# Kernel tuning notes

Hardware: AMD Instinct MI355X
Metric: run time of the kernel (lower is better)

Reference implementation:

```python
import jax, jax.numpy as jnp
import numpy as np

B, C, H, W = 2, 128, 64, 64
NUM_HEADS = 8
GN_GROUPS = 8
GN_EPS = 1e-5


def setup_inputs() -> dict:
    key = jax.random.key(0)
    ks = jax.random.split(key, 11)
    s = 0.02
    return {
        "x": jax.random.normal(ks[0], (B, C, H, W), dtype=jnp.float32),
        "Wq": jax.random.normal(ks[1], (C, C), dtype=jnp.float32) * s,
        "bq": jnp.zeros((C,), dtype=jnp.float32),
        "Wk": jax.random.normal(ks[2], (C, C), dtype=jnp.float32) * s,
        "bk": jnp.zeros((C,), dtype=jnp.float32),
        "Wv": jax.random.normal(ks[3], (C, C), dtype=jnp.float32) * s,
        "bv": jnp.zeros((C,), dtype=jnp.float32),
        "Wo": jax.random.normal(ks[4], (C, C), dtype=jnp.float32) * s,
        "bo": jnp.zeros((C,), dtype=jnp.float32),
        "gn_w": jnp.ones((C,), dtype=jnp.float32),
        "gn_b": jnp.zeros((C,), dtype=jnp.float32),
    }


def reference(x, Wq, bq, Wk, bk, Wv, bv, Wo, bo, gn_w, gn_b):
    b, c, h, w = x.shape
    nh = NUM_HEADS
    dh = c // nh
    scale = dh ** (-0.5)

    # [b, c, h, w] -> [b, N, c]
    x_seq = x.reshape(b, c, h * w).transpose(0, 2, 1)

    def proj(W, bias):
        y = jnp.einsum('bnc,dc->bnd', x_seq, W) + bias  # nn.Linear: x @ W.T + b
        return y.reshape(b, -1, nh, dh).transpose(0, 2, 1, 3)  # [b, nh, N, dh]

    q = proj(Wq, bq)
    k = proj(Wk, bk)
    v = proj(Wv, bv)

    attn = jnp.einsum('bhnd,bhmd->bhnm', q, k) * scale  # [b, nh, N, N]
    attn = jax.nn.softmax(attn, axis=-1)
    out = jnp.einsum('bhnm,bhmd->bhnd', attn, v)        # [b, nh, N, dh]

    out = out.transpose(0, 2, 1, 3).reshape(b, -1, c)   # [b, N, c]
    out = jnp.einsum('bnc,dc->bnd', out, Wo) + bo
    out = out.transpose(0, 2, 1).reshape(b, c, h, w)

    # GroupNorm(8, c) with affine params, then residual
    g = GN_GROUPS
    og = out.reshape(b, g, c // g, h, w)
    mean = jnp.mean(og, axis=(2, 3, 4), keepdims=True)
    var = jnp.var(og, axis=(2, 3, 4), keepdims=True)
    og = (og - mean) * jax.lax.rsqrt(var + GN_EPS)
    normed = og.reshape(b, c, h, w) * gn_w[None, :, None, None] + gn_b[None, :, None, None]
    return normed + x
```

## Files before the change

kernel.cpp:

```cpp
#include <hip/hip_runtime.h>

#define TID ((int)threadIdx.x)

constexpr int Bb  = 2;
constexpr int Cc  = 128;
constexpr int Nn  = 4096;
constexpr int NHh = 8;
constexpr int DHd = 16;
constexpr int NSP = 4;
constexpr float GN_EPS_F = 1e-5f;
constexpr float QSCALE = 0.25f * 1.4426950408889634f;

typedef float  f32x4  __attribute__((ext_vector_type(4)));
typedef float  f32x16 __attribute__((ext_vector_type(16)));
typedef short  s16x8  __attribute__((ext_vector_type(8)));
typedef unsigned short u16x8 __attribute__((ext_vector_type(8)));

#if __has_builtin(__builtin_amdgcn_exp2f)
#define EXP2(x) __builtin_amdgcn_exp2f(x)
#else
#define EXP2(x) exp2f(x)
#endif

constexpr size_t WS_PART = 0;
constexpr size_t WS_LP   = 4096;
constexpr size_t WS_AOP  = WS_LP + (size_t)NSP*16*Nn;
constexpr size_t WS_QBF  = WS_AOP + ((size_t)NSP*Bb*Nn*Cc)/2;
constexpr size_t BF_ELEMS = (size_t)Bb*NHh*Nn*DHd;
constexpr size_t WS_W    = WS_QBF + 3*(BF_ELEMS/2);

__device__ __forceinline__ ushort f2bf(float f) {
    uint u = __builtin_bit_cast(uint, f);
    u += 0x7fffu + ((u >> 16) & 1u);
    return (ushort)(u >> 16);
}
__device__ __forceinline__ float bf2f(ushort u) {
    return __builtin_bit_cast(float, ((uint)u) << 16);
}
__device__ __forceinline__ uint cvt_pk_bf16(float lo, float hi) {
    uint d;
    asm("v_cvt_pk_bf16_f32 %0, %1, %2" : "=v"(d) : "v"(lo), "v"(hi));
    return d;
}

__global__ __launch_bounds__(256) void prep_w_kernel(
    const float* __restrict__ Wq, const float* __restrict__ Wk,
    const float* __restrict__ Wv, const float* __restrict__ Wo,
    ushort* __restrict__ wh, ushort* __restrict__ wl)
{
    int id = blockIdx.x * 256 + TID;
    int which = id >> 14, i = id & 16383;
    const float* src = (which == 0) ? Wq : (which == 1) ? Wk : (which == 2) ? Wv : Wo;
    float v = src[i];
    if (which == 0) v *= QSCALE;
    ushort h = f2bf(v);
    ushort l = f2bf(v - bf2f(h));
    wh[id] = h;
    wl[id] = l;
}

__global__ __launch_bounds__(256) void qkv_kernel(
    const float* __restrict__ x,
    const float* __restrict__ bq, const float* __restrict__ bk, const float* __restrict__ bv,
    const ushort* __restrict__ wh, const ushort* __restrict__ wl,
    ushort* __restrict__ qbf, ushort* __restrict__ kbf, ushort* __restrict__ vtbf)
{
    const int b  = blockIdx.x >> 7;
    const int n0 = (blockIdx.x & 127) << 5;
    __shared__ __align__(16) ushort xh[32][136];
    __shared__ __align__(16) ushort xl[32][136];

    const float* xb = x + (size_t)b * Cc * Nn;
    {
        int c = TID >> 1, nh2 = (TID & 1) * 16;
#pragma unroll
        for (int j = 0; j < 4; ++j) {
            float4 v4 = *(const float4*)&xb[(size_t)c * Nn + n0 + nh2 + 4*j];
            float f[4] = {v4.x, v4.y, v4.z, v4.w};
#pragma unroll
            for (int e = 0; e < 4; ++e) {
                int n = nh2 + 4*j + e;
                ushort h = f2bf(f[e]);
                xh[n][c] = h;
                xl[n][c] = f2bf(f[e] - bf2f(h));
            }
        }
    }
    __syncthreads();

    const int lane = TID & 63, wave = TID >> 6;
    const int l31 = lane & 31, hi = lane >> 5;
    const int d0 = wave * 32;

    const ushort* wqh = wh;              const ushort* wql = wl;
    const ushort* wkh = wh + 16384;      const ushort* wkl = wl + 16384;
    const ushort* wvh = wh + 2 * 16384;  const ushort* wvl = wl + 2 * 16384;

    f32x16 qacc = (f32x16)(0.f), kacc = (f32x16)(0.f);
    f32x16 vacc = (f32x16)(bv[d0 + l31]);
    const size_t wrow = (size_t)(d0 + l31) * 128;

#pragma unroll 2
    for (int ks = 0; ks < 8; ++ks) {
        const int co = ks * 16 + 8 * hi;
        s16x8 xhf = *(const s16x8*)&xh[l31][co];
        s16x8 xlf = *(const s16x8*)&xl[l31][co];
        s16x8 aqh = *(const s16x8*)(wqh + wrow + co);
        s16x8 aql = *(const s16x8*)(wql + wrow + co);
        s16x8 akh = *(const s16x8*)(wkh + wrow + co);
        s16x8 akl = *(const s16x8*)(wkl + wrow + co);
        s16x8 avh = *(const s16x8*)(wvh + wrow + co);
        s16x8 avl = *(const s16x8*)(wvl + wrow + co);
        qacc = __builtin_amdgcn_mfma_f32_32x32x16_bf16(aqh, xhf, qacc, 0, 0, 0);
        qacc = __builtin_amdgcn_mfma_f32_32x32x16_bf16(aql, xhf, qacc, 0, 0, 0);
        qacc = __builtin_amdgcn_mfma_f32_32x32x16_bf16(aqh, xlf, qacc, 0, 0, 0);
        kacc = __builtin_amdgcn_mfma_f32_32x32x16_bf16(akh, xhf, kacc, 0, 0, 0);
        kacc = __builtin_amdgcn_mfma_f32_32x32x16_bf16(akl, xhf, kacc, 0, 0, 0);
        kacc = __builtin_amdgcn_mfma_f32_32x32x16_bf16(akh, xlf, kacc, 0, 0, 0);
        vacc = __builtin_amdgcn_mfma_f32_32x32x16_bf16(xhf, avh, vacc, 0, 0, 0);
        vacc = __builtin_amdgcn_mfma_f32_32x32x16_bf16(xhf, avl, vacc, 0, 0, 0);
        vacc = __builtin_amdgcn_mfma_f32_32x32x16_bf16(xlf, avh, vacc, 0, 0, 0);
    }

    {
        const int n = n0 + l31;
#pragma unroll
        for (int q = 0; q < 4; ++q) {
            const int dbase = d0 + 8*q + 4*hi;
            const int h = dbase >> 4, dh0 = dbase & 15;
            float4 bq4 = *(const float4*)&bq[dbase];
            float4 bk4 = *(const float4*)&bk[dbase];
            uint2 wq2, wk2;
            wq2.x = cvt_pk_bf16(qacc[4*q+0] + bq4.x * QSCALE, qacc[4*q+1] + bq4.y * QSCALE);
            wq2.y = cvt_pk_bf16(qacc[4*q+2] + bq4.z * QSCALE, qacc[4*q+3] + bq4.w * QSCALE);
            wk2.x = cvt_pk_bf16(kacc[4*q+0] + bk4.x, kacc[4*q+1] + bk4.y);
            wk2.y = cvt_pk_bf16(kacc[4*q+2] + bk4.z, kacc[4*q+3] + bk4.w);
            size_t base = ((size_t)((b*NHh + h) * Nn + n)) * DHd + dh0;
            *(uint2*)(qbf + base) = wq2;
            *(uint2*)(kbf + base) = wk2;
        }
    }
    {
        const int d = d0 + l31;
        const int h = d >> 4, dd = d & 15;
        ushort* vrow = vtbf + ((size_t)(b*NHh + h) * DHd + dd) * Nn;
#pragma unroll
        for (int q = 0; q < 4; ++q) {
            uint2 w2;
            w2.x = cvt_pk_bf16(vacc[4*q+0], vacc[4*q+1]);
            w2.y = cvt_pk_bf16(vacc[4*q+2], vacc[4*q+3]);
            *(uint2*)(vrow + n0 + 8*q + 4*hi) = w2;
        }
    }
}

__global__ __launch_bounds__(256, 5) void attn_kernel(
    const ushort* __restrict__ qbf, const ushort* __restrict__ kbf,
    const ushort* __restrict__ vtbf, ushort* __restrict__ aop, float* __restrict__ lp)
{
    const int qt = blockIdx.x & 31;
    const int sp = (blockIdx.x >> 5) & 3;
    const int bh = blockIdx.x >> 7;
    const int q0 = qt << 7;
    const int kvbase = sp << 10;
    const ushort* qb  = qbf  + (size_t)bh * Nn * DHd;
    const ushort* kb  = kbf  + (size_t)bh * Nn * DHd;
    const ushort* vtb = vtbf + (size_t)bh * DHd * Nn;

    __shared__ __align__(16) ushort k_lds[64][16];
    __shared__ __align__(16) ushort vt_lds[16][88];
    __shared__ __align__(16) ushort ps[4][32][88];

    const int wave = TID >> 6, lane = TID & 63;
    const int l31 = lane & 31, hi = lane >> 5;
    const int l15 = lane & 15, g  = lane >> 4;
    const int wq = q0 + wave * 32;

    const s16x8 qfrag = *(const s16x8*)(qb + (size_t)(wq + l31) * DHd + 8 * hi);

    float l_run = 0.0f;
    f32x4 o0 = (f32x4)(0.f), o1 = (f32x4)(0.f);
    ushort* psw = &ps[wave][0][0];

    for (int kv0 = kvbase; kv0 < kvbase + 1024; kv0 += 64) {
        if (TID < 128) {
            *(u16x8*)((char*)&k_lds[0][0] + TID * 16) =
                *(const u16x8*)(kb + (size_t)kv0 * DHd + TID * 8);
        } else {
            int t = TID - 128, r = t >> 3, c8 = (t & 7) * 8;
            *(u16x8*)&vt_lds[r][c8] = *(const u16x8*)(vtb + (size_t)r * Nn + kv0 + c8);
        }
        __syncthreads();

        s16x8 af0 = *(const s16x8*)&k_lds[l31][8 * hi];
        s16x8 af1 = *(const s16x8*)&k_lds[32 + l31][8 * hi];
        f32x16 st0 = __builtin_amdgcn_mfma_f32_32x32x16_bf16(af0, qfrag, (f32x16)(0.f), 0, 0, 0);
        f32x16 st1 = __builtin_amdgcn_mfma_f32_32x32x16_bf16(af1, qfrag, (f32x16)(0.f), 0, 0, 0);

        float rs = 0.f;
        {
            float p[16];
#pragma unroll
            for (int r = 0; r < 16; ++r) { p[r] = EXP2(st0[r]); rs += p[r]; }
            char* rowp = (char*)psw + (size_t)l31 * 176;
#pragma unroll
            for (int m4 = 0; m4 < 4; ++m4) {
                uint2 w;
                w.x = cvt_pk_bf16(p[4*m4 + 0], p[4*m4 + 1]);
                w.y = cvt_pk_bf16(p[4*m4 + 2], p[4*m4 + 3]);
                *(uint2*)(rowp + 16*m4 + 8*hi) = w;
            }
        }
        {
            float p[16];
#pragma unroll
            for (int r = 0; r < 16; ++r) { p[r] = EXP2(st1[r]); rs += p[r]; }
            char* rowp = (char*)psw + (size_t)l31 * 176;
#pragma unroll
            for (int m4 = 0; m4 < 4; ++m4) {
                uint2 w;
                w.x = cvt_pk_bf16(p[4*m4 + 0], p[4*m4 + 1]);
                w.y = cvt_pk_bf16(p[4*m4 + 2], p[4*m4 + 3]);
                *(uint2*)(rowp + 16*m4 + 8*hi + 64) = w;
            }
        }
        l_run += rs;

#pragma unroll
        for (int cc = 0; cc < 2; ++cc) {
            s16x8 vf  = *(const s16x8*)&vt_lds[l15][cc*32 + 8*g];
            s16x8 pf0 = *(const s16x8*)((char*)psw + (size_t)l15 * 176        + 16*g + 64*cc);
            s16x8 pf1 = *(const s16x8*)((char*)psw + (size_t)(16 + l15) * 176 + 16*g + 64*cc);
            o0 = __builtin_amdgcn_mfma_f32_16x16x32_bf16(pf0, vf, o0, 0, 0, 0);
            o1 = __builtin_amdgcn_mfma_f32_16x16x32_bf16(pf1, vf, o1, 0, 0, 0);
        }
        __syncthreads();
    }

    l_run += __shfl_xor(l_run, 32, 64);
    if (hi == 0)
        lp[((size_t)(sp * 16 + bh)) * Nn + wq + l31] = l_run;

    const int b = bh >> 3, hh = bh & 7;
    ushort* ap = aop + (((size_t)(sp * Bb + b)) * Nn) * Cc;
#pragma unroll
    for (int r = 0; r < 4; ++r) {
        int n0r = wq + 4*g + r, n1r = wq + 16 + 4*g + r;
        ap[(size_t)n0r * Cc + hh * DHd + l15] = f2bf(o0[r]);
        ap[(size_t)n1r * Cc + hh * DHd + l15] = f2bf(o1[r]);
    }
}

__global__ __launch_bounds__(256) void oproj_kernel(
    const ushort* __restrict__ aop, const float* __restrict__ lp,
    const ushort* __restrict__ wh, const ushort* __restrict__ wl,
    const float* __restrict__ bo,
    float* __restrict__ y, float* __restrict__ partial)
{
    const int b  = blockIdx.x >> 7;
    const int nb = blockIdx.x & 127;
    const int n0 = nb << 5;
    __shared__ __align__(16) ushort aoc[32][136];
    __shared__ float linv[32][8];

    {
        int n = TID >> 3, h = TID & 7;
        float l = 0.f;
#pragma unroll
        for (int sp = 0; sp < NSP; ++sp)
            l += lp[((size_t)(sp * 16 + b * 8 + h)) * Nn + n0 + n];
        linv[n][h] = 1.0f / l;
    }
    __syncthreads();

#pragma unroll
    for (int s = TID; s < 512; s += 256) {
        int n = s >> 4, c8 = s & 15;
        int c = c8 * 8;
        float a[8];
#pragma unroll
        for (int e = 0; e < 8; ++e) a[e] = 0.f;
#pragma unroll
        for (int sp = 0; sp < NSP; ++sp) {
            u16x8 u = *(const u16x8*)(aop + (((size_t)(sp * Bb + b)) * Nn + n0 + n) * Cc + c);
#pragma unroll
            for (int e = 0; e < 8; ++e) a[e] += bf2f(u[e]);
        }
        float li = linv[n][c >> 4];
        uint4 w;
        w.x = cvt_pk_bf16(a[0]*li, a[1]*li);
        w.y = cvt_pk_bf16(a[2]*li, a[3]*li);
        w.z = cvt_pk_bf16(a[4]*li, a[5]*li);
        w.w = cvt_pk_bf16(a[6]*li, a[7]*li);
        *(uint4*)&aoc[n][c] = w;
    }
    __syncthreads();

    const int lane = TID & 63, wave = TID >> 6;
    const int l31 = lane & 31, hi = lane >> 5;
    const int d0 = wave * 32;
    const ushort* woh = wh + 3 * 16384;
    const ushort* wol = wl + 3 * 16384;
    const size_t wrow = (size_t)(d0 + l31) * 128;

    f32x16 acc = (f32x16)(bo[d0 + l31]);
#pragma unroll
    for (int ks = 0; ks < 8; ++ks) {
        const int co = ks * 16 + 8 * hi;
        s16x8 aof = *(const s16x8*)&aoc[l31][co];
        s16x8 bh8 = *(const s16x8*)(woh + wrow + co);
        s16x8 bl8 = *(const s16x8*)(wol + wrow + co);
        acc = __builtin_amdgcn_mfma_f32_32x32x16_bf16(aof, bh8, acc, 0, 0, 0);
        acc = __builtin_amdgcn_mfma_f32_32x32x16_bf16(aof, bl8, acc, 0, 0, 0);
    }

    const int d = d0 + l31;
    float* yrow = y + ((size_t)(b * Cc + d)) * Nn + n0;
    float s1 = 0.f, s2 = 0.f;
#pragma unroll
    for (int q = 0; q < 4; ++q) {
        float4 v4 = make_float4(acc[4*q+0], acc[4*q+1], acc[4*q+2], acc[4*q+3]);
        s1 += v4.x + v4.y + v4.z + v4.w;
        s2 += v4.x*v4.x + v4.y*v4.y + v4.z*v4.z + v4.w*v4.w;
        *(float4*)(yrow + 8*q + 4*hi) = v4;
    }
#pragma unroll
    for (int off = 1; off < 16; off <<= 1) {
        s1 += __shfl_xor(s1, off, 64);
        s2 += __shfl_xor(s2, off, 64);
    }
    s1 += __shfl_xor(s1, 32, 64);
    s2 += __shfl_xor(s2, 32, 64);
    if ((lane & 15) == 0 && hi == 0) {
        int g = d >> 4;
        float* p = partial + (((size_t)(b * 128 + nb)) * 8 + g) * 2;
        p[0] = s1; p[1] = s2;
    }
}

__global__ __launch_bounds__(256) void finalize_kernel(
    const float* __restrict__ x, const float* __restrict__ gn_w, const float* __restrict__ gn_b,
    const float* __restrict__ partial, float* __restrict__ out)
{
    __shared__ float red[4][2];
    const size_t i0 = (size_t)blockIdx.x << 10;
    const int b = (int)(i0 >> 19);
    const int c = (int)((i0 >> 12) & 127);
    const int g = c >> 4;

    float s1 = 0.f, s2 = 0.f;
    if (TID < 128) {
        const float* p = partial + (((size_t)(b * 128 + TID)) * 8 + g) * 2;
        s1 = p[0]; s2 = p[1];
    }
#pragma unroll
    for (int off = 1; off < 64; off <<= 1) {
        s1 += __shfl_xor(s1, off, 64);
        s2 += __shfl_xor(s2, off, 64);
    }
    if ((TID & 63) == 0) { red[TID >> 6][0] = s1; red[TID >> 6][1] = s2; }
    __syncthreads();
    s1 = red[0][0] + red[1][0] + red[2][0] + red[3][0];
    s2 = red[0][1] + red[1][1] + red[2][1] + red[3][1];

    const float inv_cnt = 1.0f / 65536.0f;
    float mean = s1 * inv_cnt;
    float var  = s2 * inv_cnt - mean * mean;
    float rstd = rsqrtf(var + GN_EPS_F);
    float a   = rstd * gn_w[c];
    float bb2 = gn_b[c] - mean * a;

    size_t i = i0 + (size_t)TID * 4;
    float4 yv = *(float4*)(out + i);
    float4 xv = *(const float4*)(x + i);
    float4 o;
    o.x = yv.x * a + bb2 + xv.x;
    o.y = yv.y * a + bb2 + xv.y;
    o.z = yv.z * a + bb2 + xv.z;
    o.w = yv.w * a + bb2 + xv.w;
    *(float4*)(out + i) = o;
}

extern "C" void kernel_launch(void* const* d_in, const int* in_sizes, int n_in,
                              void* d_out, int out_size, void* d_ws, size_t ws_size,
                              hipStream_t stream) {
    const float* x  = (const float*)d_in[0];
    const float* Wq = (const float*)d_in[1];
    const float* bq = (const float*)d_in[2];
    const float* Wk = (const float*)d_in[3];
    const float* bk = (const float*)d_in[4];
    const float* Wv = (const float*)d_in[5];
    const float* bv = (const float*)d_in[6];
    const float* Wo = (const float*)d_in[7];
    const float* bo = (const float*)d_in[8];
    const float* gw = (const float*)d_in[9];
    const float* gb = (const float*)d_in[10];
    float* out = (float*)d_out;
    float* ws  = (float*)d_ws;

    float*  partial = ws + WS_PART;
    float*  lpart   = ws + WS_LP;
    ushort* aop     = (ushort*)(ws + WS_AOP);
    ushort* qbf     = (ushort*)(ws + WS_QBF);
    ushort* kbf     = qbf + BF_ELEMS;
    ushort* vtbf    = kbf + BF_ELEMS;
    ushort* wh      = (ushort*)(ws + WS_W);
    ushort* wl      = wh + 4 * 16384;

    hipLaunchKernelGGL(prep_w_kernel, dim3(256), dim3(256), 0, stream,
                       Wq, Wk, Wv, Wo, wh, wl);
    hipLaunchKernelGGL(qkv_kernel, dim3(Bb * (Nn / 32)), dim3(256), 0, stream,
                       x, bq, bk, bv, wh, wl, qbf, kbf, vtbf);
    hipLaunchKernelGGL(attn_kernel, dim3(16 * NSP * 32), dim3(256), 0, stream,
                       qbf, kbf, vtbf, aop, lpart);
    hipLaunchKernelGGL(oproj_kernel, dim3(Bb * (Nn / 32)), dim3(256), 0, stream,
                       aop, lpart, wh, wl, bo, out, partial);
    hipLaunchKernelGGL(finalize_kernel, dim3((Bb * Cc * Nn) / 1024), dim3(256), 0, stream,
                       x, gw, gb, partial, out);
}
```

Measured before the change: 138.7 us.

## Keep P in registers via permlane32 swap and drop LDS staging in attention

The attention kernel no longer stages K, V^T and the probability tile through shared memory. It reads K and V fragments directly from global memory, rearranges the exponentiated scores across lane halves with v_permlane32_swap, and feeds them into 32x32x16 MFMAs that accumulate the transposed output. This removes the LDS writes and reads and both __syncthreads per tile. In exchange, every wave issues redundant global and cache loads and uses more accumulator registers, so launch bounds drop from 5 to 4 blocks per CU.

```diff
diff --git a/kernel.cpp b/kernel.cpp
--- a/kernel.cpp
+++ b/kernel.cpp
@@ -15,6 +15,7 @@
 typedef float  f32x16 __attribute__((ext_vector_type(16)));
 typedef short  s16x8  __attribute__((ext_vector_type(8)));
 typedef unsigned short u16x8 __attribute__((ext_vector_type(8)));
+typedef uint   u32x4  __attribute__((ext_vector_type(4)));
 
 #if __has_builtin(__builtin_amdgcn_exp2f)
 #define EXP2(x) __builtin_amdgcn_exp2f(x)
@@ -41,6 +42,13 @@
     uint d;
     asm("v_cvt_pk_bf16_f32 %0, %1, %2" : "=v"(d) : "v"(lo), "v"(hi));
     return d;
+}
+__device__ __forceinline__ void pl32swap(uint& a, uint& b) {
+    asm volatile("v_permlane32_swap_b32 %0, %1" : "+v"(a), "+v"(b));
+}
+__device__ __forceinline__ s16x8 pack4(uint a, uint b, uint c, uint d) {
+    u32x4 u; u[0] = a; u[1] = b; u[2] = c; u[3] = d;
+    return __builtin_bit_cast(s16x8, u);
 }
 
 __global__ __launch_bounds__(256) void prep_w_kernel(
@@ -154,7 +162,7 @@
     }
 }
 
-__global__ __launch_bounds__(256, 5) void attn_kernel(
+__global__ __launch_bounds__(256, 4) void attn_kernel(
     const ushort* __restrict__ qbf, const ushort* __restrict__ kbf,
     const ushort* __restrict__ vtbf, ushort* __restrict__ aop, float* __restrict__ lp)
 {
@@ -167,74 +175,52 @@
     const ushort* kb  = kbf  + (size_t)bh * Nn * DHd;
     const ushort* vtb = vtbf + (size_t)bh * DHd * Nn;
 
-    __shared__ __align__(16) ushort k_lds[64][16];
-    __shared__ __align__(16) ushort vt_lds[16][88];
-    __shared__ __align__(16) ushort ps[4][32][88];
-
-    const int wave = TID >> 6, lane = TID & 63;
+    const int lane = TID & 63, wave = TID >> 6;
     const int l31 = lane & 31, hi = lane >> 5;
-    const int l15 = lane & 15, g  = lane >> 4;
     const int wq = q0 + wave * 32;
 
     const s16x8 qfrag = *(const s16x8*)(qb + (size_t)(wq + l31) * DHd + 8 * hi);
 
     float l_run = 0.0f;
-    f32x4 o0 = (f32x4)(0.f), o1 = (f32x4)(0.f);
-    ushort* psw = &ps[wave][0][0];
+    f32x16 ot = (f32x16)(0.f);
+
+    const ushort* vrow = vtb + (size_t)(l31 & 15) * Nn + 8 * hi;
 
     for (int kv0 = kvbase; kv0 < kvbase + 1024; kv0 += 64) {
-        if (TID < 128) {
-            *(u16x8*)((char*)&k_lds[0][0] + TID * 16) =
-                *(const u16x8*)(kb + (size_t)kv0 * DHd + TID * 8);
-        } else {
-            int t = TID - 128, r = t >> 3, c8 = (t & 7) * 8;
-            *(u16x8*)&vt_lds[r][c8] = *(const u16x8*)(vtb + (size_t)r * Nn + kv0 + c8);
-        }
-        __syncthreads();
-
-        s16x8 af0 = *(const s16x8*)&k_lds[l31][8 * hi];
-        s16x8 af1 = *(const s16x8*)&k_lds[32 + l31][8 * hi];
+        const ushort* krow = kb + (size_t)kv0 * DHd + 8 * hi;
+        s16x8 af0 = *(const s16x8*)(krow + (size_t)l31 * DHd);
+        s16x8 af1 = *(const s16x8*)(krow + (size_t)(l31 + 32) * DHd);
         f32x16 st0 = __builtin_amdgcn_mfma_f32_32x32x16_bf16(af0, qfrag, (f32x16)(0.f), 0, 0, 0);
         f32x16 st1 = __builtin_amdgcn_mfma_f32_32x32x16_bf16(af1, qfrag, (f32x16)(0.f), 0, 0, 0);
 
         float rs = 0.f;
-        {
-            float p[16];
-#pragma unroll
-            for (int r = 0; r < 16; ++r) { p[r] = EXP2(st0[r]); rs += p[r]; }
-            char* rowp = (char*)psw + (size_t)l31 * 176;
-#pragma unroll
-            for (int m4 = 0; m4 < 4; ++m4) {
-                uint2 w;
-                w.x = cvt_pk_bf16(p[4*m4 + 0], p[4*m4 + 1]);
-                w.y = cvt_pk_bf16(p[4*m4 + 2], p[4*m4 + 3]);
-                *(uint2*)(rowp + 16*m4 + 8*hi) = w;
-            }
-        }
-        {
-            float p[16];
-#pragma unroll
-            for (int r = 0; r < 16; ++r) { p[r] = EXP2(st1[r]); rs += p[r]; }
-            char* rowp = (char*)psw + (size_t)l31 * 176;
-#pragma unroll
-            for (int m4 = 0; m4 < 4; ++m4) {
-                uint2 w;
-                w.x = cvt_pk_bf16(p[4*m4 + 0], p[4*m4 + 1]);
-                w.y = cvt_pk_bf16(p[4*m4 + 2], p[4*m4 + 3]);
-                *(uint2*)(rowp + 16*m4 + 8*hi + 64) = w;
-            }
-        }
+        uint p0,p1,p2,p3,p4,p5,p6,p7,p8,p9,p10,p11,p12,p13,p14,p15;
+#define PKE(dst, sreg, i0, i1) { float e0 = EXP2(sreg[i0]); float e1 = EXP2(sreg[i1]); \
+                                 rs += e0 + e1; dst = cvt_pk_bf16(e0, e1); }
+        PKE(p0,  st0,  0,  1)  PKE(p1,  st0,  2,  3)
+        PKE(p2,  st0,  4,  5)  PKE(p3,  st0,  6,  7)
+        PKE(p4,  st0,  8,  9)  PKE(p5,  st0, 10, 11)
+        PKE(p6,  st0, 12, 13)  PKE(p7,  st0, 14, 15)
+        PKE(p8,  st1,  0,  1)  PKE(p9,  st1,  2,  3)
+        PKE(p10, st1,  4,  5)  PKE(p11, st1,  6,  7)
+        PKE(p12, st1,  8,  9)  PKE(p13, st1, 10, 11)
+        PKE(p14, st1, 12, 13)  PKE(p15, st1, 14, 15)
+#undef PKE
+        pl32swap(p0,  p2);  pl32swap(p1,  p3);
+        pl32swap(p4,  p6);  pl32swap(p5,  p7);
+        pl32swap(p8,  p10); pl32swap(p9,  p11);
+        pl32swap(p12, p14); pl32swap(p13, p15);
+
+        s16x8 vf0 = *(const s16x8*)(vrow + kv0);
+        s16x8 vf1 = *(const s16x8*)(vrow + kv0 + 16);
+        s16x8 vf2 = *(const s16x8*)(vrow + kv0 + 32);
+        s16x8 vf3 = *(const s16x8*)(vrow + kv0 + 48);
+        ot = __builtin_amdgcn_mfma_f32_32x32x16_bf16(vf0, pack4(p0,p1,p2,p3),     ot, 0, 0, 0);
+        ot = __builtin_amdgcn_mfma_f32_32x32x16_bf16(vf1, pack4(p4,p5,p6,p7),     ot, 0, 0, 0);
+        ot = __builtin_amdgcn_mfma_f32_32x32x16_bf16(vf2, pack4(p8,p9,p10,p11),   ot, 0, 0, 0);
+        ot = __builtin_amdgcn_mfma_f32_32x32x16_bf16(vf3, pack4(p12,p13,p14,p15), ot, 0, 0, 0);
+
         l_run += rs;
-
-#pragma unroll
-        for (int cc = 0; cc < 2; ++cc) {
-            s16x8 vf  = *(const s16x8*)&vt_lds[l15][cc*32 + 8*g];
-            s16x8 pf0 = *(const s16x8*)((char*)psw + (size_t)l15 * 176        + 16*g + 64*cc);
-            s16x8 pf1 = *(const s16x8*)((char*)psw + (size_t)(16 + l15) * 176 + 16*g + 64*cc);
-            o0 = __builtin_amdgcn_mfma_f32_16x16x32_bf16(pf0, vf, o0, 0, 0, 0);
-            o1 = __builtin_amdgcn_mfma_f32_16x16x32_bf16(pf1, vf, o1, 0, 0, 0);
-        }
-        __syncthreads();
     }
 
     l_run += __shfl_xor(l_run, 32, 64);
@@ -242,13 +228,12 @@
         lp[((size_t)(sp * 16 + bh)) * Nn + wq + l31] = l_run;
 
     const int b = bh >> 3, hh = bh & 7;
-    ushort* ap = aop + (((size_t)(sp * Bb + b)) * Nn) * Cc;
-#pragma unroll
-    for (int r = 0; r < 4; ++r) {
-        int n0r = wq + 4*g + r, n1r = wq + 16 + 4*g + r;
-        ap[(size_t)n0r * Cc + hh * DHd + l15] = f2bf(o0[r]);
-        ap[(size_t)n1r * Cc + hh * DHd + l15] = f2bf(o1[r]);
-    }
+    ushort* ap = aop + (((size_t)(sp * Bb + b)) * Nn + wq + l31) * Cc + hh * DHd;
+    uint2 w0, w1;
+    w0.x = cvt_pk_bf16(ot[0], ot[1]); w0.y = cvt_pk_bf16(ot[2], ot[3]);
+    w1.x = cvt_pk_bf16(ot[4], ot[5]); w1.y = cvt_pk_bf16(ot[6], ot[7]);
+    *(uint2*)(ap + 4*hi)     = w0;
+    *(uint2*)(ap + 8 + 4*hi) = w1;
 }
 
 __global__ __launch_bounds__(256) void oproj_kernel(
```

Result: slower. 172.0 us (+24.0%).
